# Kernel optimization log

Hardware: AMD Instinct MI355X
Metric: run time of the kernel (lower is better)

## Reference

```python
import jax, jax.numpy as jnp
import numpy as np

# ---- static model dims (from init_kwargs) ----
M = 128          # latent_seq_length
Mp1 = M + 1
K = 2 * Mp1      # HMM states (m,g): m in 0..M, g in {0: match, 1: insert}; k = m + (M+1)*g
D = 21           # alphabet_length
ZD = 64          # z_dim
B = 64           # batch size
L = 256          # obs_seq_length
P = Mp1 * 3 * 2  # flattened indel-parameter count (M+1, 3, 2)
NEG = -1e32      # -1/epsilon (pyro Profile epsilon=1e-32) -> forbidden transitions


def _cell_factors(n0, g, mp, gp):
    """Indel log-prob factors (param indices (m,j,s)) for a transition into state (mp,gp)
    when the next undecided ancestral slot is n0 and source type is j=g.
    j: 0=from match, 1=from insert, 2=after deletion. s: 0=no indel, 1=indel.
    Returns (insert_factors, delete_factors) or None if the transition is forbidden."""
    if mp < n0:
        return None
    rs, us = [], []
    if mp == n0:
        if gp == 0:
            rs.append((n0, g, 0)); us.append((n0, g, 0))
        else:
            rs.append((n0, g, 1))
    else:
        rs.append((n0, g, 0)); us.append((n0, g, 1))
        for mm in range(n0 + 1, mp):
            rs.append((mm, 2, 0)); us.append((mm, 2, 1))
        if gp == 0:
            rs.append((mp, 2, 0)); us.append((mp, 2, 0))
        else:
            rs.append((mp, 2, 1))
    return rs, us


def _build_tables():
    k_of = lambda m, g: m + Mp1 * g
    p_of = lambda m, j, s: (m * 3 + j) * 2 + s
    # initial-distribution transfer (dense, small): virtual source (m,g)=(-1,0) -> n0=0
    r0 = np.zeros((P, K), np.float32)
    u0 = np.zeros((P, K), np.float32)
    null0 = np.zeros((K,), np.float32)
    for mp in range(Mp1):
        for gp in range(2):
            f = _cell_factors(0, 0, mp, gp)
            kp = k_of(mp, gp)
            if f is None:
                null0[kp] = 1.0
            else:
                for t in f[0]:
                    r0[p_of(*t), kp] += 1.0
                for t in f[1]:
                    u0[p_of(*t), kp] += 1.0
    # transition-matrix transfer: sparse (param_idx, cell_idx) scatter-add lists
    r_par, r_cell, u_par, u_cell = [], [], [], []
    null = np.zeros((K, K), np.float32)
    for m in range(Mp1):
        for g in range(2):
            n0, k = m + 1 - g, k_of(m, g)
            for mp in range(Mp1):
                for gp in range(2):
                    kp = k_of(mp, gp)
                    f = _cell_factors(n0, g, mp, gp)
                    if f is None:
                        null[k, kp] = 1.0
                    else:
                        cell = k * K + kp
                        for t in f[0]:
                            r_par.append(p_of(*t)); r_cell.append(cell)
                        for t in f[1]:
                            u_par.append(p_of(*t)); u_cell.append(cell)
    return (jnp.asarray(r0), jnp.asarray(u0), jnp.asarray(null0), jnp.asarray(null),
            jnp.asarray(np.asarray(r_par, np.int32)), jnp.asarray(np.asarray(r_cell, np.int32)),
            jnp.asarray(np.asarray(u_par, np.int32)), jnp.asarray(np.asarray(u_cell, np.int32)))


R0, U0, NULL0, NULL, R_PAR, R_CELL, U_PAR, U_CELL = _build_tables()


def setup_inputs() -> dict:
    key = jax.random.key(0)
    ks = jax.random.split(key, 8)
    # variable-length one-hot sequences; missing steps are all-zero rows (pyro convention)
    tokens = jax.random.randint(ks[0], (B, L), 0, D)
    lengths = jax.random.randint(ks[1], (B,), L // 2, L + 1)
    mask = jnp.arange(L)[None, :] < lengths[:, None]
    data = jax.nn.one_hot(tokens, D, dtype=jnp.float32) * mask[:, :, None]
    z = jax.random.normal(ks[2], (B, ZD), jnp.float32)
    out_dim = 2 * Mp1 * D
    dec_W = jax.random.normal(ks[3], (out_dim, ZD), jnp.float32) / np.sqrt(ZD).astype(np.float32)
    dec_b = jax.random.normal(ks[4], (out_dim,), jnp.float32) * 0.01
    indel_prior = jnp.array([10.0, 0.0], jnp.float32)  # [strength, 0]
    insert = indel_prior + jax.random.normal(ks[5], (Mp1, 3, 2), jnp.float32)
    delete = indel_prior + jax.random.normal(ks[6], (Mp1, 3, 2), jnp.float32)
    inverse_temp = 1.0 + 0.1 * jax.random.normal(ks[7], (1,), jnp.float32)
    return {"data": data, "z": z, "dec_W": dec_W, "dec_b": dec_b,
            "insert": insert, "delete": delete, "inverse_temp": inverse_temp}


def reference(data, z, dec_W, dec_b, insert, delete, inverse_temp):
    # ---- Decoder + temperature-sharpened emission logits (FactorMuE.model) ----
    latent = (z @ dec_W.T + dec_b).reshape(-1, 2, Mp1, D)        # (B, 2, M+1, D)
    it = jax.nn.softplus(inverse_temp[0])
    anc = latent[:, 0] * it
    anc = anc - jax.nn.logsumexp(anc, axis=-1, keepdims=True)    # ancestor_seq_logits
    insq = latent[:, 1] * it
    insq = insq - jax.nn.logsumexp(insq, axis=-1, keepdims=True)  # insert_seq_logits
    ilog = insert - jax.nn.logsumexp(insert, axis=-1, keepdims=True)
    dlog = delete - jax.nn.logsumexp(delete, axis=-1, keepdims=True)
    # ---- Profile state arranger: profile-HMM -> dense HMM logits ----
    pi, pd = ilog.reshape(-1), dlog.reshape(-1)                  # (P,)
    a0 = pd @ U0 + pi @ R0 + NEG * NULL0                         # (K,) initial logits
    a = (jnp.zeros((K * K,), pi.dtype)
         .at[U_CELL].add(pd[U_PAR])
         .at[R_CELL].add(pi[R_PAR])).reshape(K, K) + NEG * NULL  # (K, K) transition logits
    e = jnp.concatenate([anc, insq], axis=1)                     # (B, K, D), k = m + (M+1)*g
    # ---- VariableLengthDiscreteHMM (MissingDataDiscreteHMM) log_prob ----
    a0 = a0 - jax.nn.logsumexp(a0)
    a = a - jax.nn.logsumexp(a, axis=-1, keepdims=True)
    e = e - jax.nn.logsumexp(e, axis=-1, keepdims=True)
    vl = jnp.einsum('bld,bkd->lbk', data, e)                     # (L, B, K); zero rows -> 0 (missing)
    alpha = a0 + vl[0]                                           # (B, K)

    def step(alpha, v):
        alpha = jax.nn.logsumexp(alpha[:, :, None] + a[None], axis=1) + v
        return alpha, None

    alpha, _ = jax.lax.scan(step, alpha, vl[1:])
    return jax.nn.logsumexp(alpha, axis=-1)                      # (B,) log-likelihood per sequence
```

## Files before the change

kernel.cpp:

```cpp
#include <hip/hip_runtime.h>
#include <math.h>

#define MP1 129
#define KK  258
#define DD  21
#define ZDIM 64
#define BB  64
#define LL  256

#define OFF_ETG  0
#define OFF_E2G  360448
#define OFF_TOK  363264
#define OFF_COEF 379648
#define C_UU   0
#define C_DXM  258
#define C_DXI  516
#define C_WM   774
#define C_WI   903
#define C_DMID 1032
#define C_PI0  1160

#define EMIS_BLKS 65
#define TOK_BLKS  1366

typedef float f32x2 __attribute__((ext_vector_type(2)));

template <int CTRL, int RM, int BM>
__device__ __forceinline__ float updpp(float old, float src) {
    return __int_as_float(__builtin_amdgcn_update_dpp(
        __float_as_int(old), __float_as_int(src), CTRL, RM, BM, false));
}
__device__ __forceinline__ float readlane_f(float v, int lane) {
    return __int_as_float(__builtin_amdgcn_readlane(__float_as_int(v), lane));
}
__device__ __forceinline__ float wave_sum_to63(float s) {
    s += updpp<0x111, 0xf, 0xf>(0.f, s);
    s += updpp<0x112, 0xf, 0xf>(0.f, s);
    s += updpp<0x114, 0xf, 0xf>(0.f, s);
    s += updpp<0x118, 0xf, 0xf>(0.f, s);
    s += updpp<0x142, 0xa, 0xf>(0.f, s);
    s += updpp<0x143, 0xc, 0xf>(0.f, s);
    return s;
}

__global__ __launch_bounds__(256, 1) void k_setup(const float* __restrict__ z,
                                                  const float* __restrict__ W,
                                                  const float* __restrict__ bias,
                                                  const float* __restrict__ invt,
                                                  const float* __restrict__ data,
                                                  const float* __restrict__ ins,
                                                  const float* __restrict__ del,
                                                  float* __restrict__ ETg,
                                                  float* __restrict__ E2g,
                                                  int* __restrict__ tokout,
                                                  float* __restrict__ coef) {
    __shared__ float il[774], dl[774], Smid[129], Qs[130];
    int bid = blockIdx.x;
    int tid = threadIdx.x;

    if (bid >= 1 && bid <= EMIS_BLKS) {
        int b  = tid & 63;
        int rr = __builtin_amdgcn_readfirstlane((bid - 1) * 4 + (tid >> 6));
        if (rr >= KK) return;
        float it = log1pf(expf(invt[0]));
        const float* wb = W + (size_t)rr * DD * ZDIM;
        const float* bp = bias + rr * DD;
        float acc[DD];
        #pragma unroll
        for (int d = 0; d < DD; ++d) acc[d] = bp[d];
        const float4* zp = (const float4*)(z + (size_t)b * ZDIM);
        #pragma unroll
        for (int c = 0; c < 4; ++c) {
            float4 za = zp[4 * c + 0], zb = zp[4 * c + 1];
            float4 zc = zp[4 * c + 2], zd = zp[4 * c + 3];
            #pragma unroll
            for (int d = 0; d < DD; ++d) {
                const float4* wp = (const float4*)(wb + (size_t)d * ZDIM + 16 * c);
                float4 wa = wp[0], wv = wp[1], wc = wp[2], wd = wp[3];
                float a = acc[d];
                a = fmaf(za.x, wa.x, a); a = fmaf(za.y, wa.y, a);
                a = fmaf(za.z, wa.z, a); a = fmaf(za.w, wa.w, a);
                a = fmaf(zb.x, wv.x, a); a = fmaf(zb.y, wv.y, a);
                a = fmaf(zb.z, wv.z, a); a = fmaf(zb.w, wv.w, a);
                a = fmaf(zc.x, wc.x, a); a = fmaf(zc.y, wc.y, a);
                a = fmaf(zc.z, wc.z, a); a = fmaf(zc.w, wc.w, a);
                a = fmaf(zd.x, wd.x, a); a = fmaf(zd.y, wd.y, a);
                a = fmaf(zd.z, wd.z, a); a = fmaf(zd.w, wd.w, a);
                acc[d] = a;
            }
        }
        float mx = acc[0] * it;
        #pragma unroll
        for (int d = 0; d < DD; ++d) { acc[d] *= it; mx = fmaxf(mx, acc[d]); }
        float s = 0.f;
        #pragma unroll
        for (int d = 0; d < DD; ++d) { acc[d] = expf(acc[d] - mx); s += acc[d]; }
        float inv = 1.0f / s;
        if (rr == 128 || rr == 257) {
            float* eb = E2g + b * 44 + ((rr == 128) ? 0 : 1);
            #pragma unroll
            for (int d = 0; d < DD; ++d) eb[d * 2] = acc[d] * inv;
            eb[DD * 2] = 1.0f;
        } else {
            bool ism = rr < 128;
            int m = ism ? rr : rr - MP1;
            int slot = (m >> 1) * 4 + (ism ? 0 : 2) + (m & 1);
            float* eb = ETg + (size_t)b * 5632 + slot;
            #pragma unroll
            for (int d = 0; d < DD; ++d) eb[d * 256] = acc[d] * inv;
            eb[DD * 256] = 1.0f;
        }
        return;
    }
    if (bid > EMIS_BLKS) {
        int wid  = (bid - 1 - EMIS_BLKS) * 4 + (tid >> 6);
        int lane = tid & 63;
        int r3   = lane / 21;
        int d    = lane - r3 * 21;
        int row  = wid * 3 + r3;
        float v = 0.f;
        if (r3 < 3 && row < BB * LL) v = data[(size_t)row * DD + d];
        unsigned long long m = __ballot(v > 0.5f);
        if (r3 < 3 && d == 0 && row < BB * LL) {
            unsigned long long slice = (m >> (21 * r3)) & 0x1FFFFFULL;
            tokout[row] = slice ? (int)__builtin_ctzll(slice) : DD;
        }
        return;
    }
    int t = tid;
    for (int p = t; p < 387; p += 256) {
        float x0 = ins[2 * p], x1 = ins[2 * p + 1];
        float mx = fmaxf(x0, x1);
        float ls = mx + logf(expf(x0 - mx) + expf(x1 - mx));
        il[2 * p] = x0 - ls; il[2 * p + 1] = x1 - ls;
        float y0 = del[2 * p], y1 = del[2 * p + 1];
        float my = fmaxf(y0, y1);
        float lt = my + logf(expf(y0 - my) + expf(y1 - my));
        dl[2 * p] = y0 - lt; dl[2 * p + 1] = y1 - lt;
    }
    __syncthreads();
    if (t < 64) {
        int mmA = 1 + 2 * t, mmB = 2 + 2 * t;
        float xA = il[(mmA * 3 + 2) * 2 + 0] + dl[(mmA * 3 + 2) * 2 + 1];
        float xB = il[(mmB * 3 + 2) * 2 + 0] + dl[(mmB * 3 + 2) * 2 + 1];
        float sc = xA + xB;
        #pragma unroll
        for (int off = 1; off < 64; off <<= 1) {
            float vv = __shfl_up(sc, off);
            if (t >= off) sc += vv;
        }
        Smid[mmB] = sc;
        Smid[mmA] = sc - xB;
        if (t == 0) Smid[0] = 0.f;
    }
    __syncthreads();
    if (t < 64) {
        int mpA = 128 - 2 * t, mpB = 127 - 2 * t;
        float aM_ = il[(mpA * 3 + 2) * 2 + 0] + dl[(mpA * 3 + 2) * 2 + 0];
        float aI_ = il[(mpA * 3 + 2) * 2 + 1];
        float mA = fmaxf(aM_, aI_);
        float pA = Smid[mpA - 1] + mA + logf(expf(aM_ - mA) + expf(aI_ - mA));
        float bM_ = il[(mpB * 3 + 2) * 2 + 0] + dl[(mpB * 3 + 2) * 2 + 0];
        float bI_ = il[(mpB * 3 + 2) * 2 + 1];
        float mB = fmaxf(bM_, bI_);
        float pB = Smid[mpB - 1] + mB + logf(expf(bM_ - mB) + expf(bI_ - mB));
        float cm = fmaxf(pA, pB);
        float cs = expf(pA - cm) + expf(pB - cm);
        #pragma unroll
        for (int off = 1; off < 64; off <<= 1) {
            float om = __shfl_up(cm, off);
            float os = __shfl_up(cs, off);
            if (t >= off) {
                float M = fmaxf(cm, om);
                cs = cs * expf(cm - M) + os * expf(om - M);
                cm = M;
            }
        }
        Qs[mpB] = cm + logf(cs);
        float em = __shfl_up(cm, 1), es = __shfl_up(cs, 1);
        if (t == 0) Qs[128] = pA;
        else {
            float M = fmaxf(em, pA);
            Qs[mpA] = M + logf(es * expf(em - M) + expf(pA - M));
        }
        if (t == 0) Qs[129] = -1e30f;
    }
    __syncthreads();
    float* uu  = coef + C_UU;
    float* dxM = coef + C_DXM;
    float* dxI = coef + C_DXI;
    float* wM  = coef + C_WM;
    float* wI  = coef + C_WI;
    float* dmd = coef + C_DMID;
    float* pi0 = coef + C_PI0;
    for (int k = t; k < KK; k += 256) {
        if (k == 128) { uu[k] = 0.f; dxM[k] = 0.f; dxI[k] = 0.f; continue; }
        int g  = (k < MP1) ? 0 : 1;
        int n0 = g ? (k - MP1) : (k + 1);
        float i0 = il[(n0 * 3 + g) * 2 + 0], i1 = il[(n0 * 3 + g) * 2 + 1];
        float e0 = dl[(n0 * 3 + g) * 2 + 0], e1 = dl[(n0 * 3 + g) * 2 + 1];
        float diagM = i0 + e0;
        float diagI = i1;
        float src   = i0 + e1;
        float tail  = src - Smid[n0] + Qs[n0 + 1];
        float M3 = fmaxf(fmaxf(diagM, diagI), tail);
        float ssum = expf(diagM - M3) + expf(diagI - M3) + expf(tail - M3);
        float lse = M3 + logf(ssum);
        uu[k]  = expf(src - lse);
        dxM[k] = expf(diagM - lse);
        dxI[k] = expf(diagI - lse);
    }
    for (int mp = t; mp < MP1; mp += 256) {
        wM[mp] = expf(il[(mp * 3 + 2) * 2 + 0] + dl[(mp * 3 + 2) * 2 + 0]);
        wI[mp] = expf(il[(mp * 3 + 2) * 2 + 1]);
    }
    for (int tt = t; tt < 128; tt += 256)
        dmd[tt] = (tt == 0) ? 1.f : expf(il[(tt * 3 + 2) * 2 + 0] + dl[(tt * 3 + 2) * 2 + 1]);
    __syncthreads();
    {
        float i00 = il[0], i01 = il[1], d00 = dl[0], d01 = dl[1];
        float a00 = i00 + d00, a0129 = i01;
        float tail0 = i00 + d01 + Qs[1];
        float M3 = fmaxf(fmaxf(a00, a0129), tail0);
        float lse0 = M3 + logf(expf(a00 - M3) + expf(a0129 - M3) + expf(tail0 - M3));
        for (int kp = t; kp < KK; kp += 256) {
            int gp = (kp >= MP1);
            int mp = gp ? (kp - MP1) : kp;
            float v;
            if (mp == 0) v = gp ? a0129 : a00;
            else v = i00 + d01 + Smid[mp - 1] +
                     (gp ? il[(mp * 3 + 2) * 2 + 1]
                         : il[(mp * 3 + 2) * 2 + 0] + dl[(mp * 3 + 2) * 2 + 0]);
            pi0[kp] = expf(v - lse0);
        }
    }
}

__global__ __launch_bounds__(64) void k_fwd(const float* __restrict__ ETg,
                                            const float* __restrict__ E2g,
                                            const int* __restrict__ tokg,
                                            const float* __restrict__ coef,
                                            float* __restrict__ out) {
    const float* uu  = coef + C_UU;
    const float* dxM = coef + C_DXM;
    const float* dxI = coef + C_DXI;
    const float* wMg = coef + C_WM;
    const float* wIg = coef + C_WI;
    const float* dmd = coef + C_DMID;
    const float* pi0 = coef + C_PI0;
    __shared__ float ETLs[22 * 256];
    int lane = threadIdx.x;
    int b = blockIdx.x;
    const float4* srcp = (const float4*)(ETg + (size_t)b * 5632);
    float4* dstp = (float4*)ETLs;
    for (int i = lane; i < 1408; i += 64) dstp[i] = srcp[i];
    float e2m = 0.f, e2i = 0.f;
    if (lane < 22) {
        e2m = E2g[b * 44 + lane * 2 + 0];
        e2i = E2g[b * 44 + lane * 2 + 1];
    }
    int4 tkv = ((const int4*)(tokg + b * LL))[lane];
    __syncthreads();

    int m0 = 2 * lane, m1 = 2 * lane + 1;
    bool L0 = (lane == 0), L63 = (lane == 63);
    float f63 = L63 ? 1.f : 0.f;
    float cM0 = L0 ? 0.f : uu[m0 - 1];
    float cM1 = uu[m0];
    f32x2 cIp  = {uu[129 + m0], uu[129 + m1]};
    float d0 = dmd[m0], d1v = dmd[m1];
    float Apair = d0 * d1v;
    f32x2 wMp  = {wMg[m0], wMg[m1]};
    f32x2 wIp  = {wIg[m0], wIg[m1]};
    f32x2 xMAp = {L0 ? 0.f : dxM[m0 - 1], dxM[m0]};
    f32x2 xIAp = {L0 ? 0.f : dxI[m0 - 1], dxI[m0]};
    f32x2 xMBp = {dxM[129 + m0], dxM[129 + m1]};
    f32x2 xIBp = {dxI[129 + m0], dxI[129 + m1]};
    f32x2 w2p  = {L63 ? wMg[128] : 0.f, L63 ? wIg[128] : 0.f};
    f32x2 xA2p = {L63 ? dxM[127] : 0.f, L63 ? dxI[127] : 0.f};
    f32x2 xB2p = {L63 ? dxM[257] : 0.f, L63 ? dxI[257] : 0.f};
    f32x2 f63p = {f63, f63};

    float A0 = Apair;
    float A1 = A0 * updpp<0x111, 0xf, 0xf>(1.f, A0);
    float A2 = A1 * updpp<0x112, 0xf, 0xf>(1.f, A1);
    float A3 = A2 * updpp<0x114, 0xf, 0xf>(1.f, A2);
    float A4 = A3 * updpp<0x118, 0xf, 0xf>(1.f, A3);
    float A5 = A4 * updpp<0x142, 0xa, 0xf>(1.f, A4);
    unsigned long long bbf = __ballot(Apair >= 1.0e-3f);
    int fast = (bbf == 0ULL);

    int lidx = lane * 4;
    int tok0 = __builtin_amdgcn_readlane(tkv.x, 0);
    float4 q0 = *(const float4*)(ETLs + tok0 * 256 + lidx);
    f32x2 e20 = {readlane_f(e2m, tok0), readlane_f(e2i, tok0)};
    f32x2 aM = {pi0[m0] * q0.x, pi0[m1] * q0.y};
    f32x2 aI = {pi0[129 + m0] * q0.z, pi0[129 + m1] * q0.w};
    f32x2 a2 = {f63 * pi0[128] * e20.x, f63 * pi0[257] * e20.y};

    int etot = 0;
    f32x2 part = (aM + aI) + a2;

    float4 q1, q2, q3, q4;
    float p2m1, p2i1, p2m2, p2i2, p2m3, p2i3, p2m4, p2i4;
#define LOADR(QN, PM, PI, TN)                                                \
    { int tn_ = (TN);                                                        \
      QN = *(const float4*)(ETLs + tn_ * 256 + lidx);                        \
      PM = readlane_f(e2m, tn_);                                             \
      PI = readlane_f(e2i, tn_); }
    LOADR(q1, p2m1, p2i1, __builtin_amdgcn_readlane(tkv.y, 0));
    LOADR(q2, p2m2, p2i2, __builtin_amdgcn_readlane(tkv.z, 0));
    LOADR(q3, p2m3, p2i3, __builtin_amdgcn_readlane(tkv.w, 0));
    LOADR(q4, p2m4, p2i4, __builtin_amdgcn_readlane(tkv.x, 1));

#define STEP_BODY(RES, PART, NL, Qr, E2M, E2I)                               \
    {                                                                        \
        f32x2 EMv = {Qr.x, Qr.y};                                            \
        f32x2 EIv = {Qr.z, Qr.w};                                            \
        f32x2 E2v = {E2M, E2I};                                              \
        if (RES) {                                                           \
            float s_ = wave_sum_to63(part.x + part.y);                       \
            float stot = readlane_f(s_, 63);                                 \
            int sb = __float_as_int(stot) & 0x7f800000;                      \
            etot += (sb >> 23);                                              \
            float invs = __int_as_float(0x7f000000 - sb);                    \
            f32x2 iv = {invs, invs};                                         \
            EMv *= iv; EIv *= iv; E2v *= iv;                                 \
        }                                                                    \
        float aMp  = updpp<0x138, 0xf, 0xf>(0.f, aM.y);        \
        float u128 = readlane_f(a2.x, 63);                                   \
        f32x2 aIc = aI * cIp;                                                \
        float r0 = fmaf(aMp, cM0, aIc.x);                                    \
        float r1 = fmaf(aM.x, cM1, aIc.y);                                   \
        float B = fmaf(d1v, r0, r1);                                         \
        B = fmaf(A0, updpp<0x111, 0xf, 0xf>(0.f, B), B);                     \
        if (NL > 1) {                                                        \
            B = fmaf(A1, updpp<0x112, 0xf, 0xf>(0.f, B), B);                 \
            B = fmaf(A2, updpp<0x114, 0xf, 0xf>(0.f, B), B);                 \
            B = fmaf(A3, updpp<0x118, 0xf, 0xf>(0.f, B), B);                 \
            B = fmaf(A4, updpp<0x142, 0xa, 0xf>(0.f, B), B);                 \
            B = fmaf(A5, updpp<0x143, 0xc, 0xf>(0.f, B), B);                 \
        }                                                                    \
        float G0 = updpp<0x138, 0xf, 0xf>(0.f, B);                           \
        float G1 = fmaf(d0, G0, r0);                                         \
        f32x2 Gp   = {G0, G1};                                               \
        f32x2 aMs  = {aMp, aM.x};                                            \
        f32x2 u2   = {u128, u128};                                           \
        f32x2 G2p  = {B, B};                                                 \
        f32x2 aM1s = {aM.y, aM.y};                                           \
        f32x2 aI2s = {a2.y, a2.y};                                           \
        f32x2 mM = wMp * Gp + (xMAp * aMs + (xMBp * aI + u2));               \
        f32x2 mI = wIp * Gp + (xIAp * aMs + (xIBp * aI + u2));               \
        f32x2 m2 = w2p * G2p + (xA2p * aM1s + (xB2p * aI2s + u2));           \
        aM = mM * EMv;                                                       \
        aI = mI * EIv;                                                       \
        a2 = m2 * E2v * f63p;                                                \
        if (PART) part = (aM + aI) + a2;                                     \
    }

#define RUN_SCAN(NL)                                                         \
    for (int it = 0; it < 63; ++it) {                                        \
        STEP_BODY(1, 0, NL, q1, p2m1, p2i1);                                 \
        LOADR(q1, p2m1, p2i1, __builtin_amdgcn_readlane(tkv.y, it + 1));     \
        STEP_BODY(0, 0, NL, q2, p2m2, p2i2);                                 \
        LOADR(q2, p2m2, p2i2, __builtin_amdgcn_readlane(tkv.z, it + 1));     \
        STEP_BODY(0, 0, NL, q3, p2m3, p2i3);                                 \
        LOADR(q3, p2m3, p2i3, __builtin_amdgcn_readlane(tkv.w, it + 1));     \
        STEP_BODY(0, 1, NL, q4, p2m4, p2i4);                                 \
        int it2 = (it + 2 < 64) ? (it + 2) : 63;                             \
        LOADR(q4, p2m4, p2i4, __builtin_amdgcn_readlane(tkv.x, it2));        \
    }                                                                        \
    STEP_BODY(1, 0, NL, q1, p2m1, p2i1);                                     \
    STEP_BODY(0, 0, NL, q2, p2m2, p2i2);                                     \
    STEP_BODY(0, 1, NL, q3, p2m3, p2i3);

    if (fast) { RUN_SCAN(1) }
    else      { RUN_SCAN(6) }
#undef RUN_SCAN
#undef STEP_BODY
#undef LOADR

    float s = wave_sum_to63(part.x + part.y);
    if (lane == 63)
        out[b] = (float)(etot - 64 * 127) * 0.6931471805599453f + logf(s);
}

extern "C" void kernel_launch(void* const* d_in, const int* in_sizes, int n_in,
                              void* d_out, int out_size, void* d_ws, size_t ws_size,
                              hipStream_t stream) {
    const float* data  = (const float*)d_in[0];
    const float* z     = (const float*)d_in[1];
    const float* dec_W = (const float*)d_in[2];
    const float* dec_b = (const float*)d_in[3];
    const float* ins   = (const float*)d_in[4];
    const float* del   = (const float*)d_in[5];
    const float* invt  = (const float*)d_in[6];
    float* out = (float*)d_out;

    float* ws   = (float*)d_ws;
    float* ETg  = ws + OFF_ETG;
    float* E2g  = ws + OFF_E2G;
    int*   tok  = (int*)(ws + OFF_TOK);
    float* coef = ws + OFF_COEF;

    k_setup<<<1 + EMIS_BLKS + TOK_BLKS, 256, 0, stream>>>(z, dec_W, dec_b, invt,
                                                          data, ins, del, ETg, E2g,
                                                          tok, coef);
    k_fwd<<<BB, 64, 0, stream>>>(ETg, E2g, tok, coef, out);
}
```

Before: 48.92 us.

## Process two batch sequences per wave in forward scan to interleave dependency chains

The forward HMM kernel now assigns two batch sequences to each 64-lane block and interleaves their scan steps. The goal is to hide the latency of the serial DPP/readlane/FMA dependency chain by giving the scheduler two independent chains. In exchange, half as many waves are launched, each doing twice the work, and register and LDS usage double per block.

```diff
diff --git a/kernel.cpp b/kernel.cpp
--- a/kernel.cpp
+++ b/kernel.cpp
@@ -248,18 +248,26 @@
     const float* wIg = coef + C_WI;
     const float* dmd = coef + C_DMID;
     const float* pi0 = coef + C_PI0;
-    __shared__ float ETLs[22 * 256];
+    __shared__ float ETLA[22 * 256];
+    __shared__ float ETLB[22 * 256];
     int lane = threadIdx.x;
-    int b = blockIdx.x;
-    const float4* srcp = (const float4*)(ETg + (size_t)b * 5632);
-    float4* dstp = (float4*)ETLs;
-    for (int i = lane; i < 1408; i += 64) dstp[i] = srcp[i];
-    float e2m = 0.f, e2i = 0.f;
+    int bA = 2 * blockIdx.x, bB = bA + 1;
+    {
+        const float4* sa = (const float4*)(ETg + (size_t)bA * 5632);
+        const float4* sb = (const float4*)(ETg + (size_t)bB * 5632);
+        float4* da = (float4*)ETLA;
+        float4* db = (float4*)ETLB;
+        for (int i = lane; i < 1408; i += 64) { da[i] = sa[i]; db[i] = sb[i]; }
+    }
+    float e2mA = 0.f, e2iA = 0.f, e2mB = 0.f, e2iB = 0.f;
     if (lane < 22) {
-        e2m = E2g[b * 44 + lane * 2 + 0];
-        e2i = E2g[b * 44 + lane * 2 + 1];
-    }
-    int4 tkv = ((const int4*)(tokg + b * LL))[lane];
+        e2mA = E2g[bA * 44 + lane * 2 + 0];
+        e2iA = E2g[bA * 44 + lane * 2 + 1];
+        e2mB = E2g[bB * 44 + lane * 2 + 0];
+        e2iB = E2g[bB * 44 + lane * 2 + 1];
+    }
+    int4 tkvA = ((const int4*)(tokg + bA * LL))[lane];
+    int4 tkvB = ((const int4*)(tokg + bB * LL))[lane];
     __syncthreads();
 
     int m0 = 2 * lane, m1 = 2 * lane + 1;
@@ -291,47 +299,59 @@
     int fast = (bbf == 0ULL);
 
     int lidx = lane * 4;
-    int tok0 = __builtin_amdgcn_readlane(tkv.x, 0);
-    float4 q0 = *(const float4*)(ETLs + tok0 * 256 + lidx);
-    f32x2 e20 = {readlane_f(e2m, tok0), readlane_f(e2i, tok0)};
-    f32x2 aM = {pi0[m0] * q0.x, pi0[m1] * q0.y};
-    f32x2 aI = {pi0[129 + m0] * q0.z, pi0[129 + m1] * q0.w};
-    f32x2 a2 = {f63 * pi0[128] * e20.x, f63 * pi0[257] * e20.y};
-
-    int etot = 0;
-    f32x2 part = (aM + aI) + a2;
-
-    float4 q1, q2, q3, q4;
-    float p2m1, p2i1, p2m2, p2i2, p2m3, p2i3, p2m4, p2i4;
-#define LOADR(QN, PM, PI, TN)                                                \
+    int tok0A = __builtin_amdgcn_readlane(tkvA.x, 0);
+    int tok0B = __builtin_amdgcn_readlane(tkvB.x, 0);
+    float4 q0A = *(const float4*)(ETLA + tok0A * 256 + lidx);
+    float4 q0B = *(const float4*)(ETLB + tok0B * 256 + lidx);
+    f32x2 aMA = {pi0[m0] * q0A.x, pi0[m1] * q0A.y};
+    f32x2 aIA = {pi0[129 + m0] * q0A.z, pi0[129 + m1] * q0A.w};
+    f32x2 a2A = {f63 * pi0[128] * readlane_f(e2mA, tok0A),
+                 f63 * pi0[257] * readlane_f(e2iA, tok0A)};
+    f32x2 aMB = {pi0[m0] * q0B.x, pi0[m1] * q0B.y};
+    f32x2 aIB = {pi0[129 + m0] * q0B.z, pi0[129 + m1] * q0B.w};
+    f32x2 a2B = {f63 * pi0[128] * readlane_f(e2mB, tok0B),
+                 f63 * pi0[257] * readlane_f(e2iB, tok0B)};
+
+    int etotA = 0, etotB = 0;
+    f32x2 partA = (aMA + aIA) + a2A;
+    f32x2 partB = (aMB + aIB) + a2B;
+
+    float4 q1A, q2A, q3A, q4A, q1B, q2B, q3B, q4B;
+    float p2m1A, p2i1A, p2m2A, p2i2A, p2m3A, p2i3A, p2m4A, p2i4A;
+    float p2m1B, p2i1B, p2m2B, p2i2B, p2m3B, p2i3B, p2m4B, p2i4B;
+#define LOADR(SFX, QN, PM, PI, TN)                                           \
     { int tn_ = (TN);                                                        \
-      QN = *(const float4*)(ETLs + tn_ * 256 + lidx);                        \
-      PM = readlane_f(e2m, tn_);                                             \
-      PI = readlane_f(e2i, tn_); }
-    LOADR(q1, p2m1, p2i1, __builtin_amdgcn_readlane(tkv.y, 0));
-    LOADR(q2, p2m2, p2i2, __builtin_amdgcn_readlane(tkv.z, 0));
-    LOADR(q3, p2m3, p2i3, __builtin_amdgcn_readlane(tkv.w, 0));
-    LOADR(q4, p2m4, p2i4, __builtin_amdgcn_readlane(tkv.x, 1));
-
-#define STEP_BODY(RES, PART, NL, Qr, E2M, E2I)                               \
+      QN = *(const float4*)(ETL##SFX + tn_ * 256 + lidx);                    \
+      PM = readlane_f(e2m##SFX, tn_);                                        \
+      PI = readlane_f(e2i##SFX, tn_); }
+    LOADR(A, q1A, p2m1A, p2i1A, __builtin_amdgcn_readlane(tkvA.y, 0));
+    LOADR(B, q1B, p2m1B, p2i1B, __builtin_amdgcn_readlane(tkvB.y, 0));
+    LOADR(A, q2A, p2m2A, p2i2A, __builtin_amdgcn_readlane(tkvA.z, 0));
+    LOADR(B, q2B, p2m2B, p2i2B, __builtin_amdgcn_readlane(tkvB.z, 0));
+    LOADR(A, q3A, p2m3A, p2i3A, __builtin_amdgcn_readlane(tkvA.w, 0));
+    LOADR(B, q3B, p2m3B, p2i3B, __builtin_amdgcn_readlane(tkvB.w, 0));
+    LOADR(A, q4A, p2m4A, p2i4A, __builtin_amdgcn_readlane(tkvA.x, 1));
+    LOADR(B, q4B, p2m4B, p2i4B, __builtin_amdgcn_readlane(tkvB.x, 1));
+
+#define STEP_BODY(SFX, RES, PART, NL, Qr, E2M, E2I)                          \
     {                                                                        \
         f32x2 EMv = {Qr.x, Qr.y};                                            \
         f32x2 EIv = {Qr.z, Qr.w};                                            \
         f32x2 E2v = {E2M, E2I};                                              \
         if (RES) {                                                           \
-            float s_ = wave_sum_to63(part.x + part.y);                       \
+            float s_ = wave_sum_to63(part##SFX.x + part##SFX.y);             \
             float stot = readlane_f(s_, 63);                                 \
             int sb = __float_as_int(stot) & 0x7f800000;                      \
-            etot += (sb >> 23);                                              \
+            etot##SFX += (sb >> 23);                                         \
             float invs = __int_as_float(0x7f000000 - sb);                    \
             f32x2 iv = {invs, invs};                                         \
             EMv *= iv; EIv *= iv; E2v *= iv;                                 \
         }                                                                    \
-        float aMp  = updpp<0x138, 0xf, 0xf>(0.f, aM.y);        \
-        float u128 = readlane_f(a2.x, 63);                                   \
-        f32x2 aIc = aI * cIp;                                                \
+        float aMp  = updpp<0x138, 0xf, 0xf>(0.f, aM##SFX.y);   \
+        float u128 = readlane_f(a2##SFX.x, 63);                              \
+        f32x2 aIc = aI##SFX * cIp;                                           \
         float r0 = fmaf(aMp, cM0, aIc.x);                                    \
-        float r1 = fmaf(aM.x, cM1, aIc.y);                                   \
+        float r1 = fmaf(aM##SFX.x, cM1, aIc.y);                              \
         float B = fmaf(d1v, r0, r1);                                         \
         B = fmaf(A0, updpp<0x111, 0xf, 0xf>(0.f, B), B);                     \
         if (NL > 1) {                                                        \
@@ -344,35 +364,46 @@
         float G0 = updpp<0x138, 0xf, 0xf>(0.f, B);                           \
         float G1 = fmaf(d0, G0, r0);                                         \
         f32x2 Gp   = {G0, G1};                                               \
-        f32x2 aMs  = {aMp, aM.x};                                            \
+        f32x2 aMs  = {aMp, aM##SFX.x};                                       \
         f32x2 u2   = {u128, u128};                                           \
         f32x2 G2p  = {B, B};                                                 \
-        f32x2 aM1s = {aM.y, aM.y};                                           \
-        f32x2 aI2s = {a2.y, a2.y};                                           \
-        f32x2 mM = wMp * Gp + (xMAp * aMs + (xMBp * aI + u2));               \
-        f32x2 mI = wIp * Gp + (xIAp * aMs + (xIBp * aI + u2));               \
+        f32x2 aM1s = {aM##SFX.y, aM##SFX.y};                                 \
+        f32x2 aI2s = {a2##SFX.y, a2##SFX.y};                                 \
+        f32x2 mM = wMp * Gp + (xMAp * aMs + (xMBp * aI##SFX + u2));          \
+        f32x2 mI = wIp * Gp + (xIAp * aMs + (xIBp * aI##SFX + u2));          \
         f32x2 m2 = w2p * G2p + (xA2p * aM1s + (xB2p * aI2s + u2));           \
-        aM = mM * EMv;                                                       \
-        aI = mI * EIv;                                                       \
-        a2 = m2 * E2v * f63p;                                                \
-        if (PART) part = (aM + aI) + a2;                                     \
+        aM##SFX = mM * EMv;                                                  \
+        aI##SFX = mI * EIv;                                                  \
+        a2##SFX = m2 * E2v * f63p;                                           \
+        if (PART) part##SFX = (aM##SFX + aI##SFX) + a2##SFX;                 \
     }
 
 #define RUN_SCAN(NL)                                                         \
     for (int it = 0; it < 63; ++it) {                                        \
-        STEP_BODY(1, 0, NL, q1, p2m1, p2i1);                                 \
-        LOADR(q1, p2m1, p2i1, __builtin_amdgcn_readlane(tkv.y, it + 1));     \
-        STEP_BODY(0, 0, NL, q2, p2m2, p2i2);                                 \
-        LOADR(q2, p2m2, p2i2, __builtin_amdgcn_readlane(tkv.z, it + 1));     \
-        STEP_BODY(0, 0, NL, q3, p2m3, p2i3);                                 \
-        LOADR(q3, p2m3, p2i3, __builtin_amdgcn_readlane(tkv.w, it + 1));     \
-        STEP_BODY(0, 1, NL, q4, p2m4, p2i4);                                 \
+        STEP_BODY(A, 1, 0, NL, q1A, p2m1A, p2i1A);                           \
+        STEP_BODY(B, 1, 0, NL, q1B, p2m1B, p2i1B);                           \
+        LOADR(A, q1A, p2m1A, p2i1A, __builtin_amdgcn_readlane(tkvA.y, it + 1)); \
+        LOADR(B, q1B, p2m1B, p2i1B, __builtin_amdgcn_readlane(tkvB.y, it + 1)); \
+        STEP_BODY(A, 0, 0, NL, q2A, p2m2A, p2i2A);                           \
+        STEP_BODY(B, 0, 0, NL, q2B, p2m2B, p2i2B);                           \
+        LOADR(A, q2A, p2m2A, p2i2A, __builtin_amdgcn_readlane(tkvA.z, it + 1)); \
+        LOADR(B, q2B, p2m2B, p2i2B, __builtin_amdgcn_readlane(tkvB.z, it + 1)); \
+        STEP_BODY(A, 0, 0, NL, q3A, p2m3A, p2i3A);                           \
+        STEP_BODY(B, 0, 0, NL, q3B, p2m3B, p2i3B);                           \
+        LOADR(A, q3A, p2m3A, p2i3A, __builtin_amdgcn_readlane(tkvA.w, it + 1)); \
+        LOADR(B, q3B, p2m3B, p2i3B, __builtin_amdgcn_readlane(tkvB.w, it + 1)); \
+        STEP_BODY(A, 0, 1, NL, q4A, p2m4A, p2i4A);                           \
+        STEP_BODY(B, 0, 1, NL, q4B, p2m4B, p2i4B);                           \
         int it2 = (it + 2 < 64) ? (it + 2) : 63;                             \
-        LOADR(q4, p2m4, p2i4, __builtin_amdgcn_readlane(tkv.x, it2));        \
+        LOADR(A, q4A, p2m4A, p2i4A, __builtin_amdgcn_readlane(tkvA.x, it2)); \
+        LOADR(B, q4B, p2m4B, p2i4B, __builtin_amdgcn_readlane(tkvB.x, it2)); \
     }                                                                        \
-    STEP_BODY(1, 0, NL, q1, p2m1, p2i1);                                     \
-    STEP_BODY(0, 0, NL, q2, p2m2, p2i2);                                     \
-    STEP_BODY(0, 1, NL, q3, p2m3, p2i3);
+    STEP_BODY(A, 1, 0, NL, q1A, p2m1A, p2i1A);                               \
+    STEP_BODY(B, 1, 0, NL, q1B, p2m1B, p2i1B);                               \
+    STEP_BODY(A, 0, 0, NL, q2A, p2m2A, p2i2A);                               \
+    STEP_BODY(B, 0, 0, NL, q2B, p2m2B, p2i2B);                               \
+    STEP_BODY(A, 0, 1, NL, q3A, p2m3A, p2i3A);                               \
+    STEP_BODY(B, 0, 1, NL, q3B, p2m3B, p2i3B);
 
     if (fast) { RUN_SCAN(1) }
     else      { RUN_SCAN(6) }
@@ -380,9 +411,12 @@
 #undef STEP_BODY
 #undef LOADR
 
-    float s = wave_sum_to63(part.x + part.y);
-    if (lane == 63)
-        out[b] = (float)(etot - 64 * 127) * 0.6931471805599453f + logf(s);
+    float sA = wave_sum_to63(partA.x + partA.y);
+    float sB = wave_sum_to63(partB.x + partB.y);
+    if (lane == 63) {
+        out[bA] = (float)(etotA - 64 * 127) * 0.6931471805599453f + logf(sA);
+        out[bB] = (float)(etotB - 64 * 127) * 0.6931471805599453f + logf(sB);
+    }
 }
 
 extern "C" void kernel_launch(void* const* d_in, const int* in_sizes, int n_in,
@@ -406,5 +440,5 @@
     k_setup<<<1 + EMIS_BLKS + TOK_BLKS, 256, 0, stream>>>(z, dec_W, dec_b, invt,
                                                           data, ins, del, ETg, E2g,
                                                           tok, coef);
-    k_fwd<<<BB, 64, 0, stream>>>(ETg, E2g, tok, coef, out);
-}
+    k_fwd<<<BB / 2, 64, 0, stream>>>(ETg, E2g, tok, coef, out);
+}
```

New measurement: 69.55 us. 42.2% more time.
